# Performance work log

Hardware: AMD Instinct MI355X
Metric: run time of the kernel (lower is better)

## Reference

```python
import jax, jax.numpy as jnp
import numpy as np
import math

NUM_CLASSES = 80
FPN_CH = 256
STEM = [256, 256, 256, 256]
C_IN = {"c3": 64, "c4": 160, "c5": 400}


def _conv(x, w, b, pad):
    # x: (B, Cin, H, W), w: (Cout, Cin, kh, kw)
    y = jax.lax.conv_general_dilated(
        x, w, window_strides=(1, 1), padding=[(pad, pad), (pad, pad)],
        dimension_numbers=("NCHW", "OIHW", "NCHW"))
    return y + b[None, :, None, None]


def _upsample2x(x):
    # F.interpolate(scale_factor=2), default mode='nearest'
    return jnp.repeat(jnp.repeat(x, 2, axis=2), 2, axis=3)


def _flatten_hw(x):
    # (B, C, H, W) -> (B, H*W, C)
    B, C, H, W = x.shape
    return x.reshape(B, C, H * W).transpose(0, 2, 1)


def setup_inputs() -> dict:
    key = jax.random.key(0)
    ks = iter(jax.random.split(key, 64))
    d = {}
    d["c3"] = jax.random.normal(next(ks), (2, 64, 64, 64), jnp.float32)
    d["c4"] = jax.random.normal(next(ks), (2, 160, 32, 32), jnp.float32)
    d["c5"] = jax.random.normal(next(ks), (2, 400, 16, 16), jnp.float32)

    def w(shape, std):
        return jax.random.normal(next(ks), shape, jnp.float32) * std

    # FPN lateral 1x1 convs and output 3x3 convs (default torch init ~ small)
    for lvl, cin in C_IN.items():
        n = lvl[1]
        d[f"lat{n}_w"] = w((FPN_CH, cin, 1, 1), 1.0 / math.sqrt(cin))
        d[f"lat{n}_b"] = jnp.zeros((FPN_CH,), jnp.float32)
        d[f"out{n}_w"] = w((FPN_CH, FPN_CH, 3, 3), 1.0 / math.sqrt(9 * FPN_CH))
        d[f"out{n}_b"] = jnp.zeros((FPN_CH,), jnp.float32)

    # Stem convs: init N(0, 0.01), bias 0 (per module code). Stacked (L, Cout, Cin, 3, 3).
    L = len(STEM)
    d["stem_cls_w"] = w((L, FPN_CH, FPN_CH, 3, 3), 0.01)
    d["stem_cls_b"] = jnp.zeros((L, FPN_CH), jnp.float32)
    d["stem_box_w"] = w((L, FPN_CH, FPN_CH, 3, 3), 0.01)
    d["stem_box_b"] = jnp.zeros((L, FPN_CH), jnp.float32)

    d["cls_w"] = w((NUM_CLASSES, FPN_CH, 3, 3), 1.0 / math.sqrt(9 * FPN_CH))
    d["cls_b"] = jnp.full((NUM_CLASSES,), -math.log(99.0), jnp.float32)
    d["box_w"] = w((4, FPN_CH, 3, 3), 1.0 / math.sqrt(9 * FPN_CH))
    d["box_b"] = jnp.zeros((4,), jnp.float32)
    d["ctr_w"] = w((1, FPN_CH, 3, 3), 1.0 / math.sqrt(9 * FPN_CH))
    d["ctr_b"] = jnp.zeros((1,), jnp.float32)
    return d


def reference(c3, c4, c5,
              lat3_w, lat3_b, lat4_w, lat4_b, lat5_w, lat5_b,
              out3_w, out3_b, out4_w, out4_b, out5_w, out5_b,
              stem_cls_w, stem_cls_b, stem_box_w, stem_box_b,
              cls_w, cls_b, box_w, box_b, ctr_w, ctr_b):
    # ---- FPN ----
    l3 = _conv(c3, lat3_w, lat3_b, 0)
    l4 = _conv(c4, lat4_w, lat4_b, 0)
    l5 = _conv(c5, lat5_w, lat5_b, 0)
    p5 = _conv(l5, out5_w, out5_b, 1)
    l4 = l4 + _upsample2x(l5)
    p4 = _conv(l4, out4_w, out4_b, 1)
    l3 = l3 + _upsample2x(l4)
    p3 = _conv(l3, out3_w, out3_b, 1)

    # ---- Prediction heads ----
    def head(feat):
        hc, hb = feat, feat
        for i in range(stem_cls_w.shape[0]):
            hc = jax.nn.relu(_conv(hc, stem_cls_w[i], stem_cls_b[i], 1))
            hb = jax.nn.relu(_conv(hb, stem_box_w[i], stem_box_b[i], 1))
        cls = _flatten_hw(_conv(hc, cls_w, cls_b, 1))      # (B, HW, num_classes)
        box = _flatten_hw(_conv(hb, box_w, box_b, 1))      # (B, HW, 4)
        ctr = _flatten_hw(_conv(hb, ctr_w, ctr_b, 1))      # (B, HW, 1)
        return cls, box, ctr

    outs = [head(p) for p in (p3, p4, p5)]
    cls_all = jnp.concatenate([o[0] for o in outs], axis=1)
    box_all = jnp.concatenate([o[1] for o in outs], axis=1)
    ctr_all = jnp.concatenate([o[2] for o in outs], axis=1)
    # pack: (B, total_locations, num_classes + 4 + 1)
    return jnp.concatenate([cls_all, box_all, ctr_all], axis=-1)
```

## Files before the change

### kernel.cpp

```cpp
#include <hip/hip_runtime.h>

typedef unsigned short u16;
typedef __attribute__((ext_vector_type(8))) __bf16 bf16x8;
typedef __attribute__((ext_vector_type(16))) float f32x16;

__device__ __forceinline__ float bf2f(u16 u) {
  union { unsigned i; float f; } x; x.i = ((unsigned)u) << 16; return x.f;
}
__device__ __forceinline__ u16 f2bf(float f) {
  union { float f; unsigned i; } x; x.f = f;
  unsigned r = x.i + 0x7FFFu + ((x.i >> 16) & 1u);
  return (u16)(r >> 16);
}
__device__ __forceinline__ bf16x8 ld8(const u16* p) {
  union { int2 i2[2]; bf16x8 v; } u;
  u.i2[0] = *(const int2*)p;
  u.i2[1] = *(const int2*)(p + 4);
  return u.v;
}

struct WJob { const float* src; u16* dst; int Cin, Cout, taps, NC, Cpad, special; };
struct WArgs {
  WJob j[16];
  const float *box_w, *ctr_w;
  const float *cls_b, *box_b, *ctr_b;
  float *bcls, *bbc;
};

__global__ __launch_bounds__(256) void wtrans_kernel(WArgs a) {
  WJob jb = a.j[blockIdx.y];
  int count = jb.taps * jb.NC * jb.Cpad * 64;
  for (int e = blockIdx.x * 256 + threadIdx.x; e < count; e += gridDim.x * 256) {
    int cw = e & 63;
    int r = e >> 6;
    int n = r % jb.Cpad;
    int q = r / jb.Cpad;
    int t = q % jb.taps;
    int cc = q / jb.taps;
    int ci = cc * 64 + cw;
    int nl = (n & ~63) + 2 * (n & 31) + ((n >> 5) & 1);
    float v = 0.f;
    if (jb.special) {
      if (ci < jb.Cin) {
        if (nl < 4) v = a.box_w[((size_t)nl * jb.Cin + ci) * jb.taps + t];
        else if (nl == 4) v = a.ctr_w[(size_t)ci * jb.taps + t];
      }
    } else if (nl < jb.Cout && ci < jb.Cin) {
      v = jb.src[((size_t)nl * jb.Cin + ci) * jb.taps + t];
    }
    jb.dst[e] = f2bf(v);
  }
  if (blockIdx.y == 0 && blockIdx.x == 0) {
    int t = threadIdx.x;
    if (t < 128) a.bcls[t] = (t < 80) ? a.cls_b[t] : 0.f;
    else if (t < 192) {
      int n = t - 128;
      a.bbc[n] = (n < 4) ? a.box_b[n] : (n == 4 ? a.ctr_b[0] : 0.f);
    }
  }
}

__global__ __launch_bounds__(256) void transpose_kernel(const float* __restrict__ c3,
                                                        const float* __restrict__ c4,
                                                        const float* __restrict__ c5,
                                                        u16* __restrict__ c3t,
                                                        u16* __restrict__ c4t,
                                                        u16* __restrict__ c5t) {
  int gid = blockIdx.x * 256 + threadIdx.x;
  const float* in; u16* out; int C, HW;
  if (gid < 524288) { in = c3; out = c3t; C = 64; HW = 4096; }
  else if (gid < 851968) { gid -= 524288; in = c4; out = c4t; C = 160; HW = 1024; }
  else { gid -= 851968; if (gid >= 204800) return; in = c5; out = c5t; C = 400; HW = 256; }
  int CHW = C * HW;
  int b = gid / CHW;
  int rem = gid - b * CHW;
  int c = rem / HW;
  int pos = rem - c * HW;
  out[((size_t)b * HW + pos) * C + c] = f2bf(in[gid]);
}

__global__ __launch_bounds__(256) void upadd2_kernel(u16* __restrict__ l3, u16* __restrict__ l4n,
                                                     const u16* __restrict__ l4,
                                                     const u16* __restrict__ l5) {
  int gid = blockIdx.x * 256 + threadIdx.x;
  if (gid < 524288) {
    int c = gid & 255; int m = gid >> 8;
    int b = m >> 10, pos = m & 1023;
    int y = pos >> 5, x = pos & 31;
    int sp = (b << 8) + ((y >> 1) << 4) + (x >> 1);
    l4n[gid] = f2bf(bf2f(l4[gid]) + bf2f(l5[(size_t)sp * 256 + c]));
  } else {
    int g2 = gid - 524288;
    int c = g2 & 255; int m = g2 >> 8;
    int b = m >> 12, pos = m & 4095;
    int y = pos >> 6, x = pos & 63;
    int sp2 = (b << 10) + ((y >> 1) << 5) + (x >> 1);
    int sp4 = (b << 8) + ((y >> 2) << 4) + (x >> 2);
    l3[g2] = f2bf(bf2f(l3[g2]) + bf2f(l4[(size_t)sp2 * 256 + c]) + bf2f(l5[(size_t)sp4 * 256 + c]));
  }
}

struct ConvP {
  const u16* src[2][3];
  const u16* wT[2][3];
  const float* bias[2][3];
  void* dst[2][3];
  int H[3], W[3], lgW[3], lgHW[3], pre[3], NC[3], Crow[3], locoff[3];
  int Cpad[2], Nvalid[2], choff[2], ny[2];
  int relu, direct;
};

#define APAD 68

#define TAPX(RB) do {                                                          \
    if (kk + 1 < ktot) {                                                       \
      writeB((kk + 1) & 1, RB);                                                \
      if (kk + 3 < ktot) loadB(kk + 3, RB);                                    \
    }                                                                          \
    int hpo = 0;                                                               \
    if (TAPS == 9) { int q_ = (t * 11) >> 5; hpo = t + 7 * q_ - 11; }          \
    const int hp = hpbase + hpo;                                               \
    const u16* ar = As + hp * APAD + koffs;                                    \
    const u16* br0 = Bs[kk & 1] + (lane & 31) * APAD + koffs;                  \
    const u16* br1 = br0 + 32 * APAD;                                          \
    _Pragma("unroll")                                                          \
    for (int ks = 0; ks < 4; ++ks) {                                           \
      bf16x8 af = ld8(ar + ks * 16);                                           \
      acc[0] = __builtin_amdgcn_mfma_f32_32x32x16_bf16(af, ld8(br0 + ks * 16), acc[0], 0, 0, 0); \
      acc[1] = __builtin_amdgcn_mfma_f32_32x32x16_bf16(af, ld8(br1 + ks * 16), acc[1], 0, 0, 0); \
    }                                                                          \
    __syncthreads();                                                           \
    ++t; ++kk;                                                                 \
    if (t == TAPS) {                                                           \
      t = 0; ++cc;                                                             \
      if (cc < NCv) {                                                          \
        writeA(rA);                                                           \
        if (cc + 1 < NCv) loadA(cc + 1, rA);                                   \
        __syncthreads();                                                       \
      }                                                                        \
    }                                                                          \
  } while (0)

template <int TAPS>
__global__ __launch_bounds__(256, 3) void conv_kernel(ConvP p) {
  constexpr int HALO_W = (TAPS == 9) ? 10 : 8;
  constexpr int HROWS = (TAPS == 9) ? 18 : 16;
  constexpr int NA = HROWS * HALO_W * 8;
  constexpr int NSLOT = (NA + 255) / 256;
  constexpr int OFF = (TAPS == 9) ? 1 : 0;
  __shared__ u16 As[180 * APAD];
  __shared__ u16 Bs[2][64 * APAD];
  const int tid = threadIdx.x;
  const int br = blockIdx.z;
  if (blockIdx.y >= p.ny[br]) return;
  const int bx = blockIdx.x;
  const int lv = (bx >= p.pre[1]) + (bx >= p.pre[2]);
  const u16* __restrict__ src = p.src[br][lv];
  const u16* __restrict__ wT = p.wT[br][lv];
  const float* bias = p.bias[br][lv];
  void* dstv = p.dst[br][lv];
  const int H = p.H[lv], W = p.W[lv];
  const int lgWv = p.lgW[lv], lgHWv = p.lgHW[lv];
  const int NCv = p.NC[lv], Crow = p.Crow[lv];
  const int Cpadv = p.Cpad[br];
  const int ktot = NCv * TAPS;
  const int nt = blockIdx.y * 64;
  const int wave = tid >> 6, lane = tid & 63;

  const int pidx = bx - p.pre[lv];
  const int lgppb = lgHWv - 7;
  const int lgnpx = lgWv - 3;
  const int batch = pidx >> lgppb;
  const int pp = pidx & ((1 << lgppb) - 1);
  const int py0 = (pp >> lgnpx) << 4;
  const int px0 = (pp & ((1 << lgnpx) - 1)) << 3;
  const size_t srcb = (size_t)batch * (1 << lgHWv) * Crow;

  f32x16 acc[2];
#pragma unroll
  for (int i = 0; i < 16; ++i) { acc[0][i] = 0.f; acc[1][i] = 0.f; }

  const int ml = wave * 32 + (lane & 31);
  const int my = ml >> 3, mx = ml & 7;
  const int koffs = (lane >> 5) << 3;
  const int hpbase = (my + OFF) * HALO_W + (mx + OFF);

  int4 rA[NSLOT];
  int4 rB0[2], rB1[2];

  auto loadA = [&](int cc2, int4* r) {
    int kb = cc2 << 6;
#pragma unroll
    for (int s = 0; s < NSLOT; ++s) {
      int idx = s * 256 + tid;
      int4 v = make_int4(0, 0, 0, 0);
      if (idx < NA) {
        int pos = idx >> 3, part = idx & 7;
        int hy = pos / HALO_W, hx = pos - hy * HALO_W;
        int gy = py0 + hy - OFF, gx = px0 + hx - OFF;
        int ch = kb + (part << 3);
        if ((unsigned)gy < (unsigned)H && (unsigned)gx < (unsigned)W && ch < Crow)
          v = *(const int4*)(src + srcb + (size_t)((gy << lgWv) + gx) * Crow + ch);
      }
      r[s] = v;
    }
  };
  auto writeA = [&](const int4* r) {
#pragma unroll
    for (int s = 0; s < NSLOT; ++s) {
      int idx = s * 256 + tid;
      if (idx < NA) {
        int pos = idx >> 3, part = idx & 7;
        u16* d = As + pos * APAD + (part << 3);
        *(int2*)d = make_int2(r[s].x, r[s].y);
        *(int2*)(d + 4) = make_int2(r[s].z, r[s].w);
      }
    }
  };
  auto loadB = [&](int j, int4* r) {
    const u16* wsrc = wT + (((size_t)j * Cpadv + nt) << 6);
    r[0] = *(const int4*)(wsrc + ((tid >> 3) << 6) + ((tid & 7) << 3));
    r[1] = *(const int4*)(wsrc + (((tid >> 3) + 32) << 6) + ((tid & 7) << 3));
  };
  auto writeB = [&](int bufi, const int4* r) {
    u16* bb = Bs[bufi];
    u16* d0 = bb + (tid >> 3) * APAD + ((tid & 7) << 3);
    u16* d1 = bb + ((tid >> 3) + 32) * APAD + ((tid & 7) << 3);
    *(int2*)d0 = make_int2(r[0].x, r[0].y);
    *(int2*)(d0 + 4) = make_int2(r[0].z, r[0].w);
    *(int2*)d1 = make_int2(r[1].x, r[1].y);
    *(int2*)(d1 + 4) = make_int2(r[1].z, r[1].w);
  };

  loadA(0, rA);
  loadB(0, rB0);
  if (ktot > 1) loadB(1, rB1);
  writeA(rA);
  writeB(0, rB0);
  if (ktot > 2) loadB(2, rB0);
  if (NCv > 1) loadA(1, rA);
  __syncthreads();

  int kk = 0, t = 0, cc = 0;
  while (true) {
    TAPX(rB1);
    if (kk >= ktot) break;
    TAPX(rB0);
    if (kk >= ktot) break;
  }

  const int col = lane & 31;
  const int rbs = 4 * (lane >> 5);
  const float bv0 = bias[nt + 2 * col];
  const float bv1 = bias[nt + 2 * col + 1];
#pragma unroll
  for (int r = 0; r < 16; ++r) {
    int m2 = wave * 32 + rbs + (r & 3) + 8 * (r >> 2);
    int posi = ((py0 + (m2 >> 3)) << lgWv) + px0 + (m2 & 7);
    float v0 = acc[0][r] + bv0;
    float v1 = acc[1][r] + bv1;
    if (p.relu) { v0 = fmaxf(v0, 0.f); v1 = fmaxf(v1, 0.f); }
    if (!p.direct) {
      unsigned pk = (unsigned)f2bf(v0) | ((unsigned)f2bf(v1) << 16);
      *(unsigned*)((u16*)dstv + ((size_t)(batch << lgHWv) + posi) * 256 + nt + 2 * col) = pk;
    } else {
      int n0 = nt + 2 * col;
      float* dd = (float*)dstv + ((size_t)(batch * 5376 + p.locoff[lv] + posi)) * 85 + p.choff[br];
      if (n0 < p.Nvalid[br]) dd[n0] = v0;
      if (n0 + 1 < p.Nvalid[br]) dd[n0 + 1] = v1;
    }
  }
}

extern "C" void kernel_launch(void* const* d_in, const int* in_sizes, int n_in,
                              void* d_out, int out_size, void* d_ws, size_t ws_size,
                              hipStream_t stream) {
  (void)in_sizes; (void)n_in; (void)out_size; (void)ws_size;
  const float* c3 = (const float*)d_in[0];
  const float* c4 = (const float*)d_in[1];
  const float* c5 = (const float*)d_in[2];
  const float* lat_w[3] = {(const float*)d_in[3], (const float*)d_in[7], (const float*)d_in[11]};
  const float* lat_b[3] = {(const float*)d_in[4], (const float*)d_in[8], (const float*)d_in[12]};
  const float* out_w[3] = {(const float*)d_in[5], (const float*)d_in[9], (const float*)d_in[13]};
  const float* out_b[3] = {(const float*)d_in[6], (const float*)d_in[10], (const float*)d_in[14]};
  const float* scw = (const float*)d_in[15];
  const float* scb = (const float*)d_in[16];
  const float* sbw = (const float*)d_in[17];
  const float* sbb = (const float*)d_in[18];
  const float* clsw = (const float*)d_in[19];
  const float* clsb = (const float*)d_in[20];
  const float* boxw = (const float*)d_in[21];
  const float* boxb = (const float*)d_in[22];
  const float* ctrw = (const float*)d_in[23];
  const float* ctrb = (const float*)d_in[24];
  float* out = (float*)d_out;
  u16* ws = (u16*)d_ws;

  size_t o = 0;
  auto alloc = [&](size_t n) { size_t r = o; o += (n + 127) & ~(size_t)127; return ws + r; };

  u16* c3t = alloc(524288);
  u16* c4t = alloc(327680);
  u16* c5t = alloc(204800);
  u16* l3 = alloc(2097152);
  u16* l4 = alloc(524288);
  u16* l4n = alloc(524288);
  u16* l5 = alloc(131072);
  u16* p3 = alloc(2097152);
  u16* p4 = alloc(524288);
  u16* p5 = alloc(131072);
  const size_t hsz[3] = {2097152, 524288, 131072};
  u16 *hc[2][3], *hb[2][3];
  for (int ab = 0; ab < 2; ++ab)
    for (int lvv = 0; lvv < 3; ++lvv) { hc[ab][lvv] = alloc(hsz[lvv]); hb[ab][lvv] = alloc(hsz[lvv]); }
  const int latCin[3] = {64, 160, 400};
  const int latNC[3] = {1, 3, 7};
  u16* wl[3]; for (int i = 0; i < 3; ++i) wl[i] = alloc((size_t)latNC[i] * 256 * 64);
  u16* wo[3]; for (int i = 0; i < 3; ++i) wo[i] = alloc(589824);
  u16* wsc[4]; for (int i = 0; i < 4; ++i) wsc[i] = alloc(589824);
  u16* wsb[4]; for (int i = 0; i < 4; ++i) wsb[i] = alloc(589824);
  u16* wcls = alloc(294912);
  u16* wbc = alloc(147456);
  float* bcls = (float*)alloc(256);
  float* bbc = (float*)alloc(128);

  WArgs wa;
  int ji = 0;
  for (int i = 0; i < 3; ++i) wa.j[ji++] = WJob{lat_w[i], wl[i], latCin[i], 256, 1, latNC[i], 256, 0};
  for (int i = 0; i < 3; ++i) wa.j[ji++] = WJob{out_w[i], wo[i], 256, 256, 9, 4, 256, 0};
  for (int i = 0; i < 4; ++i) wa.j[ji++] = WJob{scw + (size_t)i * 589824, wsc[i], 256, 256, 9, 4, 256, 0};
  for (int i = 0; i < 4; ++i) wa.j[ji++] = WJob{sbw + (size_t)i * 589824, wsb[i], 256, 256, 9, 4, 256, 0};
  wa.j[ji++] = WJob{clsw, wcls, 256, 80, 9, 4, 128, 0};
  wa.j[ji++] = WJob{nullptr, wbc, 256, 5, 9, 4, 64, 1};
  wa.box_w = boxw; wa.ctr_w = ctrw;
  wa.cls_b = clsb; wa.box_b = boxb; wa.ctr_b = ctrb; wa.bcls = bcls; wa.bbc = bbc;
  wtrans_kernel<<<dim3(96, 16), dim3(256), 0, stream>>>(wa);

  transpose_kernel<<<dim3(4128), dim3(256), 0, stream>>>(c3, c4, c5, c3t, c4t, c5t);

  const int Hs[3] = {64, 32, 16};
  const int lgWs[3] = {6, 5, 4}, lgHWs[3] = {12, 10, 8};

  auto setLv = [&](ConvP& p, int i, int lvv) {
    p.H[i] = Hs[lvv]; p.W[i] = Hs[lvv]; p.lgW[i] = lgWs[lvv]; p.lgHW[i] = lgHWs[lvv];
  };

  {
    ConvP p{};
    const u16* srcs[3] = {c3t, c4t, c5t};
    u16* dsts[3] = {l3, l4, l5};
    for (int i = 0; i < 3; ++i) {
      p.src[0][i] = srcs[i]; p.wT[0][i] = wl[i]; p.bias[0][i] = lat_b[i]; p.dst[0][i] = dsts[i];
      setLv(p, i, i);
      p.NC[i] = latNC[i]; p.Crow[i] = latCin[i]; p.locoff[i] = 0;
    }
    p.pre[0] = 0; p.pre[1] = 64; p.pre[2] = 80;
    p.Cpad[0] = 256; p.Nvalid[0] = 0; p.choff[0] = 0; p.ny[0] = 4;
    p.relu = 0; p.direct = 0;
    conv_kernel<1><<<dim3(84, 4, 1), dim3(256), 0, stream>>>(p);
  }

  upadd2_kernel<<<dim3(10240), dim3(256), 0, stream>>>(l3, l4n, l4, l5);

  {
    ConvP p{};
    const u16* srcs[3] = {l3, l4n, l5};
    u16* dsts[3] = {p3, p4, p5};
    for (int i = 0; i < 3; ++i) {
      p.src[0][i] = srcs[i]; p.wT[0][i] = wo[i]; p.bias[0][i] = out_b[i]; p.dst[0][i] = dsts[i];
      setLv(p, i, i);
      p.NC[i] = 4; p.Crow[i] = 256; p.locoff[i] = 0;
    }
    p.pre[0] = 0; p.pre[1] = 64; p.pre[2] = 80;
    p.Cpad[0] = 256; p.Nvalid[0] = 0; p.choff[0] = 0; p.ny[0] = 4;
    p.relu = 0; p.direct = 0;
    conv_kernel<9><<<dim3(84, 4, 1), dim3(256), 0, stream>>>(p);
  }

  u16* pin[3] = {p3, p4, p5};
  for (int i = 0; i < 4; ++i) {
    ConvP p{};
    int di = i & 1;
    for (int lvv = 0; lvv < 3; ++lvv) {
      const u16 *s0, *s1;
      if (i == 0) { s0 = pin[lvv]; s1 = pin[lvv]; }
      else { int si = (i - 1) & 1; s0 = hc[si][lvv]; s1 = hb[si][lvv]; }
      p.src[0][lvv] = s0; p.src[1][lvv] = s1;
      p.wT[0][lvv] = wsc[i]; p.wT[1][lvv] = wsb[i];
      p.bias[0][lvv] = scb + i * 256; p.bias[1][lvv] = sbb + i * 256;
      p.dst[0][lvv] = hc[di][lvv]; p.dst[1][lvv] = hb[di][lvv];
      setLv(p, lvv, lvv);
      p.NC[lvv] = 4; p.Crow[lvv] = 256; p.locoff[lvv] = 0;
    }
    p.pre[0] = 0; p.pre[1] = 64; p.pre[2] = 80;
    p.Cpad[0] = 256; p.Cpad[1] = 256;
    p.Nvalid[0] = 0; p.Nvalid[1] = 0; p.choff[0] = 0; p.choff[1] = 0;
    p.ny[0] = 4; p.ny[1] = 4;
    p.relu = 1; p.direct = 0;
    conv_kernel<9><<<dim3(84, 4, 2), dim3(256), 0, stream>>>(p);
  }

  {
    const int locoffs[3] = {0, 4096, 5120};
    ConvP p{};
    for (int lvv = 0; lvv < 3; ++lvv) {
      p.src[0][lvv] = hc[1][lvv]; p.wT[0][lvv] = wcls; p.bias[0][lvv] = bcls; p.dst[0][lvv] = out;
      p.src[1][lvv] = hb[1][lvv]; p.wT[1][lvv] = wbc; p.bias[1][lvv] = bbc; p.dst[1][lvv] = out;
      setLv(p, lvv, lvv);
      p.NC[lvv] = 4; p.Crow[lvv] = 256; p.locoff[lvv] = locoffs[lvv];
    }
    p.pre[0] = 0; p.pre[1] = 64; p.pre[2] = 80;
    p.Cpad[0] = 128; p.Cpad[1] = 64;
    p.Nvalid[0] = 80; p.Nvalid[1] = 5;
    p.choff[0] = 0; p.choff[1] = 80;
    p.ny[0] = 2; p.ny[1] = 1;
    p.relu = 0; p.direct = 1;
    conv_kernel<9><<<dim3(84, 2, 2), dim3(256), 0, stream>>>(p);
  }
}
```

Baseline: 366.9 us.

## Widen conv output tile to 128 channels with 2x2 wave MFMA tiling

Result: slower. 418.6 us (+14.1%).

```diff
diff --git a/kernel.cpp b/kernel.cpp
--- a/kernel.cpp
+++ b/kernel.cpp
@@ -118,38 +118,46 @@
       if (kk + 3 < ktot) loadB(kk + 3, RB);                                    \
     }                                                                          \
     int hpo = 0;                                                               \
-    if (TAPS == 9) { int q_ = (t * 11) >> 5; hpo = t + 7 * q_ - 11; }          \
+    if (TAPS == 9) { int q_ = (t * 11) >> 5; hpo = t + (HALO_W - 3) * q_ - HALO_W - 1; } \
     const int hp = hpbase + hpo;                                               \
     const u16* ar = As + hp * APAD + koffs;                                    \
-    const u16* br0 = Bs[kk & 1] + (lane & 31) * APAD + koffs;                  \
-    const u16* br1 = br0 + 32 * APAD;                                          \
+    const u16* brn = Bs[kk & 1] + bro;                                         \
     _Pragma("unroll")                                                          \
     for (int ks = 0; ks < 4; ++ks) {                                           \
-      bf16x8 af = ld8(ar + ks * 16);                                           \
-      acc[0] = __builtin_amdgcn_mfma_f32_32x32x16_bf16(af, ld8(br0 + ks * 16), acc[0], 0, 0, 0); \
-      acc[1] = __builtin_amdgcn_mfma_f32_32x32x16_bf16(af, ld8(br1 + ks * 16), acc[1], 0, 0, 0); \
+      bf16x8 b0 = ld8(brn + ks * 16);                                          \
+      bf16x8 b1 = ld8(brn + 32 * APAD + ks * 16);                              \
+      bf16x8 a0 = ld8(ar + ks * 16);                                           \
+      acc[0][0] = __builtin_amdgcn_mfma_f32_32x32x16_bf16(a0, b0, acc[0][0], 0, 0, 0); \
+      acc[0][1] = __builtin_amdgcn_mfma_f32_32x32x16_bf16(a0, b1, acc[0][1], 0, 0, 0); \
+      if (FM == 2) {                                                           \
+        bf16x8 a1 = ld8(ar + 4 * HALO_W * APAD + ks * 16);                     \
+        acc[FM - 1][0] = __builtin_amdgcn_mfma_f32_32x32x16_bf16(a1, b0, acc[FM - 1][0], 0, 0, 0); \
+        acc[FM - 1][1] = __builtin_amdgcn_mfma_f32_32x32x16_bf16(a1, b1, acc[FM - 1][1], 0, 0, 0); \
+      }                                                                        \
     }                                                                          \
     __syncthreads();                                                           \
     ++t; ++kk;                                                                 \
     if (t == TAPS) {                                                           \
       t = 0; ++cc;                                                             \
       if (cc < NCv) {                                                          \
-        writeA(rA);                                                           \
+        writeA(rA);                                                            \
         if (cc + 1 < NCv) loadA(cc + 1, rA);                                   \
         __syncthreads();                                                       \
       }                                                                        \
     }                                                                          \
   } while (0)
 
-template <int TAPS>
-__global__ __launch_bounds__(256, 3) void conv_kernel(ConvP p) {
+template <int TAPS, int WN>
+__global__ __launch_bounds__(256, 2) void conv_kernel(ConvP p) {
   constexpr int HALO_W = (TAPS == 9) ? 10 : 8;
   constexpr int HROWS = (TAPS == 9) ? 18 : 16;
   constexpr int NA = HROWS * HALO_W * 8;
   constexpr int NSLOT = (NA + 255) / 256;
   constexpr int OFF = (TAPS == 9) ? 1 : 0;
+  constexpr int FM = WN;
+  constexpr int NB = 2 * WN;
   __shared__ u16 As[180 * APAD];
-  __shared__ u16 Bs[2][64 * APAD];
+  __shared__ u16 Bs[2][64 * WN * APAD];
   const int tid = threadIdx.x;
   const int br = blockIdx.z;
   if (blockIdx.y >= p.ny[br]) return;
@@ -164,8 +172,10 @@
   const int NCv = p.NC[lv], Crow = p.Crow[lv];
   const int Cpadv = p.Cpad[br];
   const int ktot = NCv * TAPS;
-  const int nt = blockIdx.y * 64;
+  const int nt = blockIdx.y * (WN * 64);
   const int wave = tid >> 6, lane = tid & 63;
+  const int mi = (WN == 2) ? (wave & 1) : wave;
+  const int ni = (WN == 2) ? (wave >> 1) : 0;
 
   const int pidx = bx - p.pre[lv];
   const int lgppb = lgHWv - 7;
@@ -176,17 +186,20 @@
   const int px0 = (pp & ((1 << lgnpx) - 1)) << 3;
   const size_t srcb = (size_t)batch * (1 << lgHWv) * Crow;
 
-  f32x16 acc[2];
-#pragma unroll
-  for (int i = 0; i < 16; ++i) { acc[0][i] = 0.f; acc[1][i] = 0.f; }
-
-  const int ml = wave * 32 + (lane & 31);
-  const int my = ml >> 3, mx = ml & 7;
+  f32x16 acc[FM][2];
+#pragma unroll
+  for (int fm = 0; fm < FM; ++fm)
+#pragma unroll
+    for (int i = 0; i < 16; ++i) { acc[fm][0][i] = 0.f; acc[fm][1][i] = 0.f; }
+
+  const int ml0 = ((WN == 2) ? mi * 64 : wave * 32) + (lane & 31);
+  const int my = ml0 >> 3, mx = ml0 & 7;
   const int koffs = (lane >> 5) << 3;
   const int hpbase = (my + OFF) * HALO_W + (mx + OFF);
+  const int bro = ((lane & 31) + ni * 64) * APAD + koffs;
 
   int4 rA[NSLOT];
-  int4 rB0[2], rB1[2];
+  int4 rB0[NB], rB1[NB];
 
   auto loadA = [&](int cc2, int4* r) {
     int kb = cc2 << 6;
@@ -219,17 +232,21 @@
   };
   auto loadB = [&](int j, int4* r) {
     const u16* wsrc = wT + (((size_t)j * Cpadv + nt) << 6);
-    r[0] = *(const int4*)(wsrc + ((tid >> 3) << 6) + ((tid & 7) << 3));
-    r[1] = *(const int4*)(wsrc + (((tid >> 3) + 32) << 6) + ((tid & 7) << 3));
+#pragma unroll
+    for (int s = 0; s < NB; ++s) {
+      int idx = s * 256 + tid;
+      r[s] = *(const int4*)(wsrc + ((idx >> 3) << 6) + ((idx & 7) << 3));
+    }
   };
   auto writeB = [&](int bufi, const int4* r) {
     u16* bb = Bs[bufi];
-    u16* d0 = bb + (tid >> 3) * APAD + ((tid & 7) << 3);
-    u16* d1 = bb + ((tid >> 3) + 32) * APAD + ((tid & 7) << 3);
-    *(int2*)d0 = make_int2(r[0].x, r[0].y);
-    *(int2*)(d0 + 4) = make_int2(r[0].z, r[0].w);
-    *(int2*)d1 = make_int2(r[1].x, r[1].y);
-    *(int2*)(d1 + 4) = make_int2(r[1].z, r[1].w);
+#pragma unroll
+    for (int s = 0; s < NB; ++s) {
+      int idx = s * 256 + tid;
+      u16* d = bb + (idx >> 3) * APAD + ((idx & 7) << 3);
+      *(int2*)d = make_int2(r[s].x, r[s].y);
+      *(int2*)(d + 4) = make_int2(r[s].z, r[s].w);
+    }
   };
 
   loadA(0, rA);
@@ -251,23 +268,27 @@
 
   const int col = lane & 31;
   const int rbs = 4 * (lane >> 5);
-  const float bv0 = bias[nt + 2 * col];
-  const float bv1 = bias[nt + 2 * col + 1];
-#pragma unroll
-  for (int r = 0; r < 16; ++r) {
-    int m2 = wave * 32 + rbs + (r & 3) + 8 * (r >> 2);
-    int posi = ((py0 + (m2 >> 3)) << lgWv) + px0 + (m2 & 7);
-    float v0 = acc[0][r] + bv0;
-    float v1 = acc[1][r] + bv1;
-    if (p.relu) { v0 = fmaxf(v0, 0.f); v1 = fmaxf(v1, 0.f); }
-    if (!p.direct) {
-      unsigned pk = (unsigned)f2bf(v0) | ((unsigned)f2bf(v1) << 16);
-      *(unsigned*)((u16*)dstv + ((size_t)(batch << lgHWv) + posi) * 256 + nt + 2 * col) = pk;
-    } else {
-      int n0 = nt + 2 * col;
-      float* dd = (float*)dstv + ((size_t)(batch * 5376 + p.locoff[lv] + posi)) * 85 + p.choff[br];
-      if (n0 < p.Nvalid[br]) dd[n0] = v0;
-      if (n0 + 1 < p.Nvalid[br]) dd[n0 + 1] = v1;
+  const int nbase = nt + ni * 64 + 2 * col;
+  const float bv0 = bias[nbase];
+  const float bv1 = bias[nbase + 1];
+#pragma unroll
+  for (int fm = 0; fm < FM; ++fm) {
+    const int mbase = ((WN == 2) ? mi * 64 + fm * 32 : wave * 32);
+#pragma unroll
+    for (int r = 0; r < 16; ++r) {
+      int m2 = mbase + rbs + (r & 3) + 8 * (r >> 2);
+      int posi = ((py0 + (m2 >> 3)) << lgWv) + px0 + (m2 & 7);
+      float v0 = acc[fm][0][r] + bv0;
+      float v1 = acc[fm][1][r] + bv1;
+      if (p.relu) { v0 = fmaxf(v0, 0.f); v1 = fmaxf(v1, 0.f); }
+      if (!p.direct) {
+        unsigned pk = (unsigned)f2bf(v0) | ((unsigned)f2bf(v1) << 16);
+        *(unsigned*)((u16*)dstv + ((size_t)(batch << lgHWv) + posi) * 256 + nbase) = pk;
+      } else {
+        float* dd = (float*)dstv + ((size_t)(batch * 5376 + p.locoff[lv] + posi)) * 85 + p.choff[br];
+        if (nbase < p.Nvalid[br]) dd[nbase] = v0;
+        if (nbase + 1 < p.Nvalid[br]) dd[nbase + 1] = v1;
+      }
     }
   }
 }
@@ -355,9 +376,9 @@
       p.NC[i] = latNC[i]; p.Crow[i] = latCin[i]; p.locoff[i] = 0;
     }
     p.pre[0] = 0; p.pre[1] = 64; p.pre[2] = 80;
-    p.Cpad[0] = 256; p.Nvalid[0] = 0; p.choff[0] = 0; p.ny[0] = 4;
+    p.Cpad[0] = 256; p.Nvalid[0] = 0; p.choff[0] = 0; p.ny[0] = 2;
     p.relu = 0; p.direct = 0;
-    conv_kernel<1><<<dim3(84, 4, 1), dim3(256), 0, stream>>>(p);
+    conv_kernel<1, 2><<<dim3(84, 2, 1), dim3(256), 0, stream>>>(p);
   }
 
   upadd2_kernel<<<dim3(10240), dim3(256), 0, stream>>>(l3, l4n, l4, l5);
@@ -372,9 +393,9 @@
       p.NC[i] = 4; p.Crow[i] = 256; p.locoff[i] = 0;
     }
     p.pre[0] = 0; p.pre[1] = 64; p.pre[2] = 80;
-    p.Cpad[0] = 256; p.Nvalid[0] = 0; p.choff[0] = 0; p.ny[0] = 4;
+    p.Cpad[0] = 256; p.Nvalid[0] = 0; p.choff[0] = 0; p.ny[0] = 2;
     p.relu = 0; p.direct = 0;
-    conv_kernel<9><<<dim3(84, 4, 1), dim3(256), 0, stream>>>(p);
+    conv_kernel<9, 2><<<dim3(84, 2, 1), dim3(256), 0, stream>>>(p);
   }
 
   u16* pin[3] = {p3, p4, p5};
@@ -395,26 +416,34 @@
     p.pre[0] = 0; p.pre[1] = 64; p.pre[2] = 80;
     p.Cpad[0] = 256; p.Cpad[1] = 256;
     p.Nvalid[0] = 0; p.Nvalid[1] = 0; p.choff[0] = 0; p.choff[1] = 0;
-    p.ny[0] = 4; p.ny[1] = 4;
+    p.ny[0] = 2; p.ny[1] = 2;
     p.relu = 1; p.direct = 0;
-    conv_kernel<9><<<dim3(84, 4, 2), dim3(256), 0, stream>>>(p);
-  }
-
+    conv_kernel<9, 2><<<dim3(84, 2, 2), dim3(256), 0, stream>>>(p);
+  }
+
+  const int locoffs[3] = {0, 4096, 5120};
   {
-    const int locoffs[3] = {0, 4096, 5120};
     ConvP p{};
     for (int lvv = 0; lvv < 3; ++lvv) {
       p.src[0][lvv] = hc[1][lvv]; p.wT[0][lvv] = wcls; p.bias[0][lvv] = bcls; p.dst[0][lvv] = out;
-      p.src[1][lvv] = hb[1][lvv]; p.wT[1][lvv] = wbc; p.bias[1][lvv] = bbc; p.dst[1][lvv] = out;
       setLv(p, lvv, lvv);
       p.NC[lvv] = 4; p.Crow[lvv] = 256; p.locoff[lvv] = locoffs[lvv];
     }
     p.pre[0] = 0; p.pre[1] = 64; p.pre[2] = 80;
-    p.Cpad[0] = 128; p.Cpad[1] = 64;
-    p.Nvalid[0] = 80; p.Nvalid[1] = 5;
-    p.choff[0] = 0; p.choff[1] = 80;
-    p.ny[0] = 2; p.ny[1] = 1;
+    p.Cpad[0] = 128; p.Nvalid[0] = 80; p.choff[0] = 0; p.ny[0] = 1;
     p.relu = 0; p.direct = 1;
-    conv_kernel<9><<<dim3(84, 2, 2), dim3(256), 0, stream>>>(p);
-  }
-}
+    conv_kernel<9, 2><<<dim3(84, 1, 1), dim3(256), 0, stream>>>(p);
+  }
+  {
+    ConvP p{};
+    for (int lvv = 0; lvv < 3; ++lvv) {
+      p.src[0][lvv] = hb[1][lvv]; p.wT[0][lvv] = wbc; p.bias[0][lvv] = bbc; p.dst[0][lvv] = out;
+      setLv(p, lvv, lvv);
+      p.NC[lvv] = 4; p.Crow[lvv] = 256; p.locoff[lvv] = locoffs[lvv];
+    }
+    p.pre[0] = 0; p.pre[1] = 64; p.pre[2] = 80;
+    p.Cpad[0] = 64; p.Nvalid[0] = 5; p.choff[0] = 80; p.ny[0] = 1;
+    p.relu = 0; p.direct = 1;
+    conv_kernel<9, 1><<<dim3(84, 1, 1), dim3(256), 0, stream>>>(p);
+  }
+}
```

## Replace LDS-staged 3x3 conv with register-direct global loads per tap

Applied to the files above, without the earlier changes.

New measurement: 779.0 us. +112.3%, slower.

```diff
diff --git a/kernel.cpp b/kernel.cpp
--- a/kernel.cpp
+++ b/kernel.cpp
@@ -18,8 +18,11 @@
   u.i2[1] = *(const int2*)(p + 4);
   return u.v;
 }
-
-struct WJob { const float* src; u16* dst; int Cin, Cout, taps, NC, Cpad, special; };
+__device__ __forceinline__ bf16x8 as_bf(int4 v) {
+  union { int4 i; bf16x8 b; } u; u.i = v; return u.b;
+}
+
+struct WJob { const float* src; u16* dst; int Cin, Cout, taps, NC, Cpad, special, lgw; };
 struct WArgs {
   WJob j[16];
   const float *box_w, *ctr_w;
@@ -29,15 +32,16 @@
 
 __global__ __launch_bounds__(256) void wtrans_kernel(WArgs a) {
   WJob jb = a.j[blockIdx.y];
-  int count = jb.taps * jb.NC * jb.Cpad * 64;
+  int wide = 1 << jb.lgw;
+  int count = jb.taps * jb.NC * jb.Cpad * wide;
   for (int e = blockIdx.x * 256 + threadIdx.x; e < count; e += gridDim.x * 256) {
-    int cw = e & 63;
-    int r = e >> 6;
+    int cw = e & (wide - 1);
+    int r = e >> jb.lgw;
     int n = r % jb.Cpad;
     int q = r / jb.Cpad;
     int t = q % jb.taps;
     int cc = q / jb.taps;
-    int ci = cc * 64 + cw;
+    int ci = cc * wide + cw;
     int nl = (n & ~63) + 2 * (n & 31) + ((n >> 5) & 1);
     float v = 0.f;
     if (jb.special) {
@@ -117,9 +121,7 @@
       writeB((kk + 1) & 1, RB);                                                \
       if (kk + 3 < ktot) loadB(kk + 3, RB);                                    \
     }                                                                          \
-    int hpo = 0;                                                               \
-    if (TAPS == 9) { int q_ = (t * 11) >> 5; hpo = t + 7 * q_ - 11; }          \
-    const int hp = hpbase + hpo;                                               \
+    const int hp = hpbase;                                                     \
     const u16* ar = As + hp * APAD + koffs;                                    \
     const u16* br0 = Bs[kk & 1] + (lane & 31) * APAD + koffs;                  \
     const u16* br1 = br0 + 32 * APAD;                                          \
@@ -130,25 +132,20 @@
       acc[1] = __builtin_amdgcn_mfma_f32_32x32x16_bf16(af, ld8(br1 + ks * 16), acc[1], 0, 0, 0); \
     }                                                                          \
     __syncthreads();                                                           \
-    ++t; ++kk;                                                                 \
-    if (t == TAPS) {                                                           \
-      t = 0; ++cc;                                                             \
-      if (cc < NCv) {                                                          \
-        writeA(rA);                                                           \
-        if (cc + 1 < NCv) loadA(cc + 1, rA);                                   \
-        __syncthreads();                                                       \
-      }                                                                        \
+    ++kk; ++cc;                                                                \
+    if (cc < NCv) {                                                            \
+      writeA(rA);                                                              \
+      if (cc + 1 < NCv) loadA(cc + 1, rA);                                     \
+      __syncthreads();                                                         \
     }                                                                          \
   } while (0)
 
-template <int TAPS>
-__global__ __launch_bounds__(256, 3) void conv_kernel(ConvP p) {
-  constexpr int HALO_W = (TAPS == 9) ? 10 : 8;
-  constexpr int HROWS = (TAPS == 9) ? 18 : 16;
+__global__ __launch_bounds__(256, 3) void conv1_kernel(ConvP p) {
+  constexpr int HALO_W = 8;
+  constexpr int HROWS = 16;
   constexpr int NA = HROWS * HALO_W * 8;
   constexpr int NSLOT = (NA + 255) / 256;
-  constexpr int OFF = (TAPS == 9) ? 1 : 0;
-  __shared__ u16 As[180 * APAD];
+  __shared__ u16 As[128 * APAD];
   __shared__ u16 Bs[2][64 * APAD];
   const int tid = threadIdx.x;
   const int br = blockIdx.z;
@@ -163,7 +160,7 @@
   const int lgWv = p.lgW[lv], lgHWv = p.lgHW[lv];
   const int NCv = p.NC[lv], Crow = p.Crow[lv];
   const int Cpadv = p.Cpad[br];
-  const int ktot = NCv * TAPS;
+  const int ktot = NCv;
   const int nt = blockIdx.y * 64;
   const int wave = tid >> 6, lane = tid & 63;
 
@@ -183,7 +180,7 @@
   const int ml = wave * 32 + (lane & 31);
   const int my = ml >> 3, mx = ml & 7;
   const int koffs = (lane >> 5) << 3;
-  const int hpbase = (my + OFF) * HALO_W + (mx + OFF);
+  const int hpbase = my * HALO_W + mx;
 
   int4 rA[NSLOT];
   int4 rB0[2], rB1[2];
@@ -197,7 +194,7 @@
       if (idx < NA) {
         int pos = idx >> 3, part = idx & 7;
         int hy = pos / HALO_W, hx = pos - hy * HALO_W;
-        int gy = py0 + hy - OFF, gx = px0 + hx - OFF;
+        int gy = py0 + hy, gx = px0 + hx;
         int ch = kb + (part << 3);
         if ((unsigned)gy < (unsigned)H && (unsigned)gx < (unsigned)W && ch < Crow)
           v = *(const int4*)(src + srcb + (size_t)((gy << lgWv) + gx) * Crow + ch);
@@ -241,7 +238,7 @@
   if (NCv > 1) loadA(1, rA);
   __syncthreads();
 
-  int kk = 0, t = 0, cc = 0;
+  int kk = 0, cc = 0;
   while (true) {
     TAPX(rB1);
     if (kk >= ktot) break;
@@ -253,6 +250,125 @@
   const int rbs = 4 * (lane >> 5);
   const float bv0 = bias[nt + 2 * col];
   const float bv1 = bias[nt + 2 * col + 1];
+#pragma unroll
+  for (int r = 0; r < 16; ++r) {
+    int m2 = wave * 32 + rbs + (r & 3) + 8 * (r >> 2);
+    int posi = ((py0 + (m2 >> 3)) << lgWv) + px0 + (m2 & 7);
+    float v0 = acc[0][r] + bv0;
+    float v1 = acc[1][r] + bv1;
+    unsigned pk = (unsigned)f2bf(v0) | ((unsigned)f2bf(v1) << 16);
+    *(unsigned*)((u16*)dstv + ((size_t)(batch << lgHWv) + posi) * 256 + nt + 2 * col) = pk;
+  }
+}
+
+struct ConvP9 {
+  const u16* src[2][3];
+  const u16* wT[2][3];
+  const float* bias[2][3];
+  void* dst[2][3];
+  int H[3], W[3], lgW[3], lgHW[3], pre[3], locoff[3];
+  int Cpad[2], Nvalid[2], choff[2], ny[2];
+  int relu, direct;
+};
+
+#define LDA2(T, CH) do {                                                       \
+    const u16* ap_ = src + srcb + aoff[T] + (CH) * 32;                         \
+    int4 va_ = *(const int4*)ap_;                                              \
+    int4 vb_ = *(const int4*)(ap_ + 16);                                       \
+    if (!(avalid & (1u << (T)))) { va_ = izero; vb_ = izero; }                 \
+    rAa[T] = va_; rAb[T] = vb_;                                                \
+  } while (0)
+
+#define LDB9(KK, RB) do {                                                      \
+    const u16* bp_ = wT + (size_t)(KK) * (Cpadv << 5) + bo0;                   \
+    RB[0] = *(const int4*)bp_;                                                 \
+    RB[1] = *(const int4*)(bp_ + 16);                                          \
+    RB[2] = *(const int4*)(bp_ + 1024);                                        \
+    RB[3] = *(const int4*)(bp_ + 1040);                                        \
+  } while (0)
+
+#define TAPU(T, CH, RB) do {                                                   \
+    bf16x8 a0_ = as_bf(rAa[T]);                                                \
+    bf16x8 a1_ = as_bf(rAb[T]);                                                \
+    acc[0] = __builtin_amdgcn_mfma_f32_32x32x16_bf16(a0_, as_bf(RB[0]), acc[0], 0, 0, 0); \
+    acc[1] = __builtin_amdgcn_mfma_f32_32x32x16_bf16(a0_, as_bf(RB[2]), acc[1], 0, 0, 0); \
+    acc[0] = __builtin_amdgcn_mfma_f32_32x32x16_bf16(a1_, as_bf(RB[1]), acc[0], 0, 0, 0); \
+    acc[1] = __builtin_amdgcn_mfma_f32_32x32x16_bf16(a1_, as_bf(RB[3]), acc[1], 0, 0, 0); \
+    if ((CH) < 7) LDA2(T, (CH) + 1);                                           \
+    int kn_ = (CH) * 9 + (T) + 2;                                              \
+    if (kn_ < 72) LDB9(kn_, RB);                                               \
+  } while (0)
+
+__global__ __launch_bounds__(256, 2) void conv9r_kernel(ConvP9 p) {
+  const int tid = threadIdx.x;
+  const int br = blockIdx.z;
+  if (blockIdx.y >= p.ny[br]) return;
+  const int bx = blockIdx.x;
+  const int lv = (bx >= p.pre[1]) + (bx >= p.pre[2]);
+  const u16* __restrict__ src = p.src[br][lv];
+  const u16* __restrict__ wT = p.wT[br][lv];
+  const float* bias = p.bias[br][lv];
+  void* dstv = p.dst[br][lv];
+  const int H = p.H[lv], W = p.W[lv];
+  const int lgWv = p.lgW[lv], lgHWv = p.lgHW[lv];
+  const int Cpadv = p.Cpad[br];
+  const int nt = blockIdx.y * 64;
+  const int wave = tid >> 6, lane = tid & 63;
+  const int khalf = lane >> 5;
+
+  const int pidx = bx - p.pre[lv];
+  const int lgppb = lgHWv - 7;
+  const int lgnpx = lgWv - 3;
+  const int batch = pidx >> lgppb;
+  const int pp = pidx & ((1 << lgppb) - 1);
+  const int py0 = (pp >> lgnpx) << 4;
+  const int px0 = (pp & ((1 << lgnpx) - 1)) << 3;
+  const size_t srcb = (size_t)batch << (lgHWv + 8);
+
+  const int ml = wave * 32 + (lane & 31);
+  const int my = ml >> 3, mx = ml & 7;
+  const int bo0 = ((nt + (lane & 31)) << 5) + khalf * 8;
+
+  const int4 izero = make_int4(0, 0, 0, 0);
+  int aoff[9];
+  unsigned avalid = 0;
+#pragma unroll
+  for (int dy = -1; dy <= 1; ++dy)
+#pragma unroll
+    for (int dx = -1; dx <= 1; ++dx) {
+      int pI = (dy + 1) * 3 + (dx + 1);
+      int y = py0 + my + dy, x = px0 + mx + dx;
+      bool v = ((unsigned)y < (unsigned)H) && ((unsigned)x < (unsigned)W);
+      int yc = v ? y : 0, xc = v ? x : 0;
+      aoff[pI] = (((yc << lgWv) + xc) << 8) + khalf * 8;
+      if (v) avalid |= 1u << pI;
+    }
+
+  f32x16 acc[2];
+#pragma unroll
+  for (int i = 0; i < 16; ++i) { acc[0][i] = 0.f; acc[1][i] = 0.f; }
+
+  int4 rAa[9], rAb[9], rB0[4], rB1[4];
+#pragma unroll
+  for (int t = 0; t < 9; ++t) LDA2(t, 0);
+  LDB9(0, rB0);
+  LDB9(1, rB1);
+
+  for (int cp = 0; cp < 4; ++cp) {
+    const int c0 = cp * 2;
+    TAPU(0, c0, rB0); TAPU(1, c0, rB1); TAPU(2, c0, rB0);
+    TAPU(3, c0, rB1); TAPU(4, c0, rB0); TAPU(5, c0, rB1);
+    TAPU(6, c0, rB0); TAPU(7, c0, rB1); TAPU(8, c0, rB0);
+    TAPU(0, c0 + 1, rB1); TAPU(1, c0 + 1, rB0); TAPU(2, c0 + 1, rB1);
+    TAPU(3, c0 + 1, rB0); TAPU(4, c0 + 1, rB1); TAPU(5, c0 + 1, rB0);
+    TAPU(6, c0 + 1, rB1); TAPU(7, c0 + 1, rB0); TAPU(8, c0 + 1, rB1);
+  }
+
+  const int col = lane & 31;
+  const int rbs = 4 * (lane >> 5);
+  const int nbase = nt + 2 * col;
+  const float bv0 = bias[nbase];
+  const float bv1 = bias[nbase + 1];
 #pragma unroll
   for (int r = 0; r < 16; ++r) {
     int m2 = wave * 32 + rbs + (r & 3) + 8 * (r >> 2);
@@ -262,12 +378,11 @@
     if (p.relu) { v0 = fmaxf(v0, 0.f); v1 = fmaxf(v1, 0.f); }
     if (!p.direct) {
       unsigned pk = (unsigned)f2bf(v0) | ((unsigned)f2bf(v1) << 16);
-      *(unsigned*)((u16*)dstv + ((size_t)(batch << lgHWv) + posi) * 256 + nt + 2 * col) = pk;
+      *(unsigned*)((u16*)dstv + ((size_t)(batch << lgHWv) + posi) * 256 + nbase) = pk;
     } else {
-      int n0 = nt + 2 * col;
       float* dd = (float*)dstv + ((size_t)(batch * 5376 + p.locoff[lv] + posi)) * 85 + p.choff[br];
-      if (n0 < p.Nvalid[br]) dd[n0] = v0;
-      if (n0 + 1 < p.Nvalid[br]) dd[n0 + 1] = v1;
+      if (nbase < p.Nvalid[br]) dd[nbase] = v0;
+      if (nbase + 1 < p.Nvalid[br]) dd[nbase + 1] = v1;
     }
   }
 }
@@ -323,15 +438,16 @@
   u16* wbc = alloc(147456);
   float* bcls = (float*)alloc(256);
   float* bbc = (float*)alloc(128);
+  alloc(2048);
 
   WArgs wa;
   int ji = 0;
-  for (int i = 0; i < 3; ++i) wa.j[ji++] = WJob{lat_w[i], wl[i], latCin[i], 256, 1, latNC[i], 256, 0};
-  for (int i = 0; i < 3; ++i) wa.j[ji++] = WJob{out_w[i], wo[i], 256, 256, 9, 4, 256, 0};
-  for (int i = 0; i < 4; ++i) wa.j[ji++] = WJob{scw + (size_t)i * 589824, wsc[i], 256, 256, 9, 4, 256, 0};
-  for (int i = 0; i < 4; ++i) wa.j[ji++] = WJob{sbw + (size_t)i * 589824, wsb[i], 256, 256, 9, 4, 256, 0};
-  wa.j[ji++] = WJob{clsw, wcls, 256, 80, 9, 4, 128, 0};
-  wa.j[ji++] = WJob{nullptr, wbc, 256, 5, 9, 4, 64, 1};
+  for (int i = 0; i < 3; ++i) wa.j[ji++] = WJob{lat_w[i], wl[i], latCin[i], 256, 1, latNC[i], 256, 0, 6};
+  for (int i = 0; i < 3; ++i) wa.j[ji++] = WJob{out_w[i], wo[i], 256, 256, 9, 8, 256, 0, 5};
+  for (int i = 0; i < 4; ++i) wa.j[ji++] = WJob{scw + (size_t)i * 589824, wsc[i], 256, 256, 9, 8, 256, 0, 5};
+  for (int i = 0; i < 4; ++i) wa.j[ji++] = WJob{sbw + (size_t)i * 589824, wsb[i], 256, 256, 9, 8, 256, 0, 5};
+  wa.j[ji++] = WJob{clsw, wcls, 256, 80, 9, 8, 128, 0, 5};
+  wa.j[ji++] = WJob{nullptr, wbc, 256, 5, 9, 8, 64, 1, 5};
   wa.box_w = boxw; wa.ctr_w = ctrw;
   wa.cls_b = clsb; wa.box_b = boxb; wa.ctr_b = ctrb; wa.bcls = bcls; wa.bbc = bbc;
   wtrans_kernel<<<dim3(96, 16), dim3(256), 0, stream>>>(wa);
@@ -340,10 +456,6 @@
 
   const int Hs[3] = {64, 32, 16};
   const int lgWs[3] = {6, 5, 4}, lgHWs[3] = {12, 10, 8};
-
-  auto setLv = [&](ConvP& p, int i, int lvv) {
-    p.H[i] = Hs[lvv]; p.W[i] = Hs[lvv]; p.lgW[i] = lgWs[lvv]; p.lgHW[i] = lgHWs[lvv];
-  };
 
   {
     ConvP p{};
@@ -351,35 +463,38 @@
     u16* dsts[3] = {l3, l4, l5};
     for (int i = 0; i < 3; ++i) {
       p.src[0][i] = srcs[i]; p.wT[0][i] = wl[i]; p.bias[0][i] = lat_b[i]; p.dst[0][i] = dsts[i];
-      setLv(p, i, i);
+      p.H[i] = Hs[i]; p.W[i] = Hs[i]; p.lgW[i] = lgWs[i]; p.lgHW[i] = lgHWs[i];
       p.NC[i] = latNC[i]; p.Crow[i] = latCin[i]; p.locoff[i] = 0;
     }
     p.pre[0] = 0; p.pre[1] = 64; p.pre[2] = 80;
     p.Cpad[0] = 256; p.Nvalid[0] = 0; p.choff[0] = 0; p.ny[0] = 4;
     p.relu = 0; p.direct = 0;
-    conv_kernel<1><<<dim3(84, 4, 1), dim3(256), 0, stream>>>(p);
+    conv1_kernel<<<dim3(84, 4, 1), dim3(256), 0, stream>>>(p);
   }
 
   upadd2_kernel<<<dim3(10240), dim3(256), 0, stream>>>(l3, l4n, l4, l5);
 
+  auto setLv9 = [&](ConvP9& p, int i) {
+    p.H[i] = Hs[i]; p.W[i] = Hs[i]; p.lgW[i] = lgWs[i]; p.lgHW[i] = lgHWs[i];
+  };
+
   {
-    ConvP p{};
+    ConvP9 p{};
     const u16* srcs[3] = {l3, l4n, l5};
     u16* dsts[3] = {p3, p4, p5};
     for (int i = 0; i < 3; ++i) {
       p.src[0][i] = srcs[i]; p.wT[0][i] = wo[i]; p.bias[0][i] = out_b[i]; p.dst[0][i] = dsts[i];
-      setLv(p, i, i);
-      p.NC[i] = 4; p.Crow[i] = 256; p.locoff[i] = 0;
+      setLv9(p, i); p.locoff[i] = 0;
     }
     p.pre[0] = 0; p.pre[1] = 64; p.pre[2] = 80;
     p.Cpad[0] = 256; p.Nvalid[0] = 0; p.choff[0] = 0; p.ny[0] = 4;
     p.relu = 0; p.direct = 0;
-    conv_kernel<9><<<dim3(84, 4, 1), dim3(256), 0, stream>>>(p);
+    conv9r_kernel<<<dim3(84, 4, 1), dim3(256), 0, stream>>>(p);
   }
 
   u16* pin[3] = {p3, p4, p5};
   for (int i = 0; i < 4; ++i) {
-    ConvP p{};
+    ConvP9 p{};
     int di = i & 1;
     for (int lvv = 0; lvv < 3; ++lvv) {
       const u16 *s0, *s1;
@@ -389,25 +504,23 @@
       p.wT[0][lvv] = wsc[i]; p.wT[1][lvv] = wsb[i];
       p.bias[0][lvv] = scb + i * 256; p.bias[1][lvv] = sbb + i * 256;
       p.dst[0][lvv] = hc[di][lvv]; p.dst[1][lvv] = hb[di][lvv];
-      setLv(p, lvv, lvv);
-      p.NC[lvv] = 4; p.Crow[lvv] = 256; p.locoff[lvv] = 0;
+      setLv9(p, lvv); p.locoff[lvv] = 0;
     }
     p.pre[0] = 0; p.pre[1] = 64; p.pre[2] = 80;
     p.Cpad[0] = 256; p.Cpad[1] = 256;
     p.Nvalid[0] = 0; p.Nvalid[1] = 0; p.choff[0] = 0; p.choff[1] = 0;
     p.ny[0] = 4; p.ny[1] = 4;
     p.relu = 1; p.direct = 0;
-    conv_kernel<9><<<dim3(84, 4, 2), dim3(256), 0, stream>>>(p);
+    conv9r_kernel<<<dim3(84, 4, 2), dim3(256), 0, stream>>>(p);
   }
 
   {
     const int locoffs[3] = {0, 4096, 5120};
-    ConvP p{};
+    ConvP9 p{};
     for (int lvv = 0; lvv < 3; ++lvv) {
       p.src[0][lvv] = hc[1][lvv]; p.wT[0][lvv] = wcls; p.bias[0][lvv] = bcls; p.dst[0][lvv] = out;
       p.src[1][lvv] = hb[1][lvv]; p.wT[1][lvv] = wbc; p.bias[1][lvv] = bbc; p.dst[1][lvv] = out;
-      setLv(p, lvv, lvv);
-      p.NC[lvv] = 4; p.Crow[lvv] = 256; p.locoff[lvv] = locoffs[lvv];
+      setLv9(p, lvv); p.locoff[lvv] = locoffs[lvv];
     }
     p.pre[0] = 0; p.pre[1] = 64; p.pre[2] = 80;
     p.Cpad[0] = 128; p.Cpad[1] = 64;
@@ -415,6 +528,6 @@
     p.choff[0] = 0; p.choff[1] = 80;
     p.ny[0] = 2; p.ny[1] = 1;
     p.relu = 0; p.direct = 1;
-    conv_kernel<9><<<dim3(84, 2, 2), dim3(256), 0, stream>>>(p);
-  }
-}
+    conv9r_kernel<<<dim3(84, 2, 2), dim3(256), 0, stream>>>(p);
+  }
+}
```
